# Optimization experiments

Hardware: AMD Instinct MI355X
Metric: run time of the kernel (lower is better)

The kernel has to match this reference:

```python
import jax, jax.numpy as jnp
import numpy as np

IMAGE_SIZE = 256
NEAR = 0.1
FAR = 100.0
CHUNK = 200  # faces per rasterization chunk


def setup_inputs() -> dict:
    key = jax.random.key(0)
    k1, k2, k3 = jax.random.split(key, 3)
    B, Nv, Nf = 1, 10000, 10000
    # vertices sized so that after weak projection (u = f*x + c, f=1015, c=112,
    # orig_size=224) they land inside the image plane; z kept positive.
    xy = jax.random.uniform(k1, (B, Nv, 2), minval=-0.1, maxval=0.1)
    z = jax.random.uniform(k3, (B, Nv, 1), minval=0.4, maxval=0.8)
    vertices = jnp.concatenate([xy, z], axis=-1).astype(jnp.float32)
    faces = jax.random.randint(k2, (B, Nf, 3), 0, Nv).astype(jnp.int64)
    f, c = 1015.0, 112.0
    K = jnp.broadcast_to(jnp.array([[f, 0.0, c], [0.0, f, c], [0.0, 0.0, 1.0]],
                                   dtype=jnp.float32), (B, 3, 3))
    R = jnp.broadcast_to(jnp.eye(3, dtype=jnp.float32), (B, 3, 3))
    t = jnp.zeros((B, 3), dtype=jnp.float32)
    return {"vertices": vertices, "faces": faces, "K": K, "R": R, "t": t,
            "orig_size": 224}


def weak_projection(vertices, K, R, t, orig_size):
    # camera transform: v_cam = v @ R^T + t   [B,N,3]
    v = jnp.einsum('bnj,bkj->bnk', vertices, R) + t[:, None, :]
    x, y, z = v[..., 0], v[..., 1], v[..., 2]
    fx, fy = K[:, 0:1, 0], K[:, 1:2, 1]  # [B,1]
    cx, cy = K[:, 0:1, 2], K[:, 1:2, 2]
    # weak (orthographic-with-focal) projection: no divide by z
    u = fx * x + cx
    w = fy * y + cy
    xn = 2.0 * u / orig_size - 1.0        # NDC x in [-1,1]
    yn = -(2.0 * w / orig_size - 1.0)     # image y down -> NDC y up
    return jnp.stack([xn, yn, z], axis=-1)


def _rasterize_depth(face_verts):
    # face_verts: [B, F, 3, 3] (NDC x, NDC y, camera z)
    B, F = face_verts.shape[0], face_verts.shape[1]
    IS = IMAGE_SIZE
    ps = (2.0 * (jnp.arange(IS, dtype=jnp.float32) + 0.5) / IS) - 1.0
    px = ps[None, :]    # [1, W]
    py = -ps[:, None]   # [H, 1], row 0 is top of image

    def chunk_depth(fc):  # fc: [B, C, 3, 3] -> per-pixel min depth [B, H, W]
        x = fc[..., 0][..., None, None]  # [B,C,3,1,1]
        y = fc[..., 1][..., None, None]
        z = fc[..., 2]                   # [B,C,3]
        dx0, dx1, dx2 = x[:, :, 0] - px, x[:, :, 1] - px, x[:, :, 2] - px  # [B,C,1,W]
        dy0, dy1, dy2 = y[:, :, 0] - py, y[:, :, 1] - py, y[:, :, 2] - py  # [B,C,H,1]
        # edge functions (unnormalized barycentric weights) [B,C,H,W]
        w0 = dx1 * dy2 - dx2 * dy1
        w1 = dx2 * dy0 - dx0 * dy2
        w2 = dx0 * dy1 - dx1 * dy0
        area = w0 + w1 + w2
        s = jnp.sign(area)
        inside = (w0 * s >= 0) & (w1 * s >= 0) & (w2 * s >= 0) & (jnp.abs(area) > 1e-10)
        safe_area = jnp.where(jnp.abs(area) > 1e-10, area, 1.0)
        zp = (w0 * z[:, :, 0, None, None] + w1 * z[:, :, 1, None, None]
              + w2 * z[:, :, 2, None, None]) / safe_area
        valid = inside & (zp > NEAR) & (zp < FAR)
        return jnp.min(jnp.where(valid, zp, FAR), axis=1)  # [B,H,W]

    pad = (-F) % CHUNK
    fv = jnp.pad(face_verts, ((0, 0), (0, pad), (0, 0), (0, 0)))  # degenerate pads -> area 0
    n = (F + pad) // CHUNK
    fv = fv.reshape(B, n, CHUNK, 3, 3).transpose(1, 0, 2, 3, 4)  # [n,B,C,3,3]
    ck = jax.checkpoint(chunk_depth)

    def step(carry, fc):
        return jnp.minimum(carry, ck(fc)), None

    depth0 = jnp.full((B, IS, IS), FAR, dtype=jnp.float32)
    depth, _ = jax.lax.scan(step, depth0, fv)
    return depth


def reference(vertices, faces, K, R, t, orig_size):
    # fill_back: append reversed-winding copies of every face
    faces2 = jnp.concatenate([faces, faces[:, :, ::-1]], axis=1)  # [B,2F,3]
    v = weak_projection(vertices, K, R, t, orig_size)             # [B,Nv,3]
    face_verts = jax.vmap(lambda vb, fb: vb[fb])(v, faces2)       # [B,2F,3,3]
    return _rasterize_depth(face_verts)                           # [B,256,256]
```

## Files before the change

### kernel.cpp

```cpp
#include <hip/hip_runtime.h>

#define IMG 256
#define FARZ 100.0f
#define FARB 0x42C80000u
#define TILE 16
#define NZ 4
#define RND 256
#define EPS 1e-4f
#define EPSZ 1e-5f
#define DPIX (2.0f / IMG)

typedef float f2 __attribute__((ext_vector_type(2)));
static __device__ __forceinline__ f2 pkfma(f2 a, f2 b, f2 c) {
    return __builtin_elementwise_fma(a, b, c);
}
static __device__ __forceinline__ float wave_max(float v) {
#pragma unroll
    for (int m = 32; m >= 1; m >>= 1) v = fmaxf(v, __shfl_xor(v, m, 64));
    return v;
}
static __device__ __forceinline__ float wave_min(float v) {
#pragma unroll
    for (int m = 32; m >= 1; m >>= 1) v = fminf(v, __shfl_xor(v, m, 64));
    return v;
}

struct Q4 { f2 r0, r1; };
static __device__ __forceinline__ Q4 eval4(float A, float B, float C,
                                           float px0, float py0) {
    Q4 o;
    float w00 = fmaf(B, px0, fmaf(C, py0, A));
    o.r0 = pkfma((f2){B, B}, (f2){0.0f, DPIX}, (f2){w00, w00});
    o.r1 = pkfma((f2){C, C}, (f2){-DPIX, -DPIX}, o.r0);
    return o;
}

__global__ __launch_bounds__(256) void setup(const float* __restrict__ verts,
                                             const int* __restrict__ faces,
                                             const float* __restrict__ K,
                                             const float* __restrict__ Rm,
                                             const float* __restrict__ t,
                                             const int* __restrict__ osz,
                                             float4* __restrict__ Q0,
                                             float4* __restrict__ Q1,
                                             float4* __restrict__ Q2,
                                             float4* __restrict__ BB,
                                             unsigned* __restrict__ gb,
                                             unsigned* __restrict__ out, int Nf) {
    __shared__ float sb[4][4];
    int tid = threadIdx.x;
    int i = blockIdx.x * 256 + tid;
    out[i] = FARB;

    float k0 = 104.0f, k1 = 104.0f, k2 = 104.0f, k3 = 104.0f;

    if (i < Nf) {
        float fx = K[0], cx = K[2], fy = K[4], cy = K[5];
        float os = (float)osz[0];
        float r00 = Rm[0], r01 = Rm[1], r02 = Rm[2];
        float r10 = Rm[3], r11 = Rm[4], r12 = Rm[5];
        float r20 = Rm[6], r21 = Rm[7], r22 = Rm[8];
        float t0 = t[0], t1 = t[1], t2 = t[2];

        float3 p[3];
#pragma unroll
        for (int k = 0; k < 3; ++k) {
            int vi = faces[3 * i + k];
            float vx = verts[3 * vi], vy = verts[3 * vi + 1], vz = verts[3 * vi + 2];
            float x = r00 * vx + r01 * vy + r02 * vz + t0;
            float y = r10 * vx + r11 * vy + r12 * vz + t1;
            float z = r20 * vx + r21 * vy + r22 * vz + t2;
            float u = fx * x + cx;
            float w = fy * y + cy;
            p[k].x = 2.0f * u / os - 1.0f;
            p[k].y = -(2.0f * w / os - 1.0f);
            p[k].z = z;
        }

        float xmn = fminf(p[0].x, fminf(p[1].x, p[2].x));
        float xmx = fmaxf(p[0].x, fmaxf(p[1].x, p[2].x));
        float ymn = fminf(p[0].y, fminf(p[1].y, p[2].y));
        float ymx = fmaxf(p[0].y, fmaxf(p[1].y, p[2].y));
        k0 = 4.0f + xmn; k1 = 4.0f - xmx; k2 = 4.0f + ymn; k3 = 4.0f - ymx;

        float A0 = p[1].x * p[2].y - p[2].x * p[1].y;
        float B0 = p[1].y - p[2].y;
        float C0 = p[2].x - p[1].x;
        float A1 = p[2].x * p[0].y - p[0].x * p[2].y;
        float B1 = p[2].y - p[0].y;
        float C1 = p[0].x - p[2].x;
        float A2 = p[0].x * p[1].y - p[1].x * p[0].y;
        float B2 = p[0].y - p[1].y;
        float C2 = p[1].x - p[0].x;

        float area = A0 + A1 + A2;
        if (fabsf(area) > 1e-10f) {
            float s = (area > 0.0f) ? 1.0f : -1.0f;
            A0 *= s; B0 *= s; C0 *= s;
            A1 *= s; B1 *= s; C1 *= s;
            A2 *= s; B2 *= s; C2 *= s;
            float inv = (1.0f / area) * s;
            float P = (A0 * p[0].z + A1 * p[1].z + A2 * p[2].z) * inv;
            float Q = (B0 * p[0].z + B1 * p[1].z + B2 * p[2].z) * inv;
            float Rr = (C0 * p[0].z + C1 * p[1].z + C2 * p[2].z) * inv;
            Q0[i] = make_float4(A0, B0, C0, A1);
            Q1[i] = make_float4(B1, C1, A2, B2);
            Q2[i] = make_float4(C2, P, Q, Rr);
            BB[i] = make_float4(xmn, xmx, ymn, ymx);
        } else {
            Q0[i] = make_float4(0.0f, 0.0f, 0.0f, 0.0f);
            Q1[i] = make_float4(0.0f, 0.0f, 0.0f, 0.0f);
            Q2[i] = make_float4(0.0f, 0.0f, 0.0f, 0.0f);
            BB[i] = make_float4(2.0f, 2.0f, 2.0f, 2.0f);
        }
    }

    k0 = wave_min(k0); k1 = wave_min(k1); k2 = wave_min(k2); k3 = wave_min(k3);
    int wave = tid >> 6, lane = tid & 63;
    if (lane == 0) { sb[wave][0] = k0; sb[wave][1] = k1; sb[wave][2] = k2; sb[wave][3] = k3; }
    __syncthreads();
    if (tid < 4) {
        float v = fminf(fminf(sb[0][tid], sb[1][tid]), fminf(sb[2][tid], sb[3][tid]));
        atomicMin(&gb[tid], __float_as_uint(v));
    }
}

__global__ __launch_bounds__(256) void raster(const float4* __restrict__ Q0,
                                              const float4* __restrict__ Q1,
                                              const float4* __restrict__ Q2,
                                              const float4* __restrict__ BB,
                                              const unsigned* __restrict__ gb,
                                              unsigned* __restrict__ out,
                                              int Nf, int span) {
    __shared__ float4 sf[RND * 3];
    __shared__ unsigned sdepth[TILE * TILE];
    __shared__ float swr[4];
    __shared__ int scnt;

    const int tid = threadIdx.x;
    const int bx = blockIdx.x, by = blockIdx.y;
    const int wave = tid >> 6, lane = tid & 63;

    const float cx0 = -1.0f + (bx * TILE + 0.5f) * DPIX;
    const float cx1 = cx0 + (TILE - 1) * DPIX;
    const float cyTop = 1.0f - (by * TILE + 0.5f) * DPIX;
    const float cyBot = cyTop - (TILE - 1) * DPIX;
    const float tcx = 0.5f * (cx0 + cx1);
    const float tcy = 0.5f * (cyBot + cyTop);
    const float hx = 0.5f * (cx1 - cx0);
    const float hy = 0.5f * (cyTop - cyBot);

    const float gxmin = __uint_as_float(gb[0]) - 4.0f;
    const float gxmax = 4.0f - __uint_as_float(gb[1]);
    const float gymin = __uint_as_float(gb[2]) - 4.0f;
    const float gymax = 4.0f - __uint_as_float(gb[3]);

    const int col = tid & 15, row = tid >> 4;
    const float pxt = cx0 + (float)col * DPIX;
    const float pyt = cyTop - (float)row * DPIX;
    const bool coverable = (pxt >= gxmin - 1e-6f) & (pxt <= gxmax + 1e-6f) &
                           (pyt >= gymin - 1e-6f) & (pyt <= gymax + 1e-6f);
    const int gidx = (by * TILE + row) * IMG + bx * TILE + col;
    const unsigned orig = out[gidx];
    sdepth[tid] = orig;
    if (tid == 0) scnt = 0;
    {
        float v = coverable ? __uint_as_float(orig) : 0.0f;
        float wm = wave_max(v);
        if (lane == 0) swr[wave] = wm;
    }
    __syncthreads();
    float T = fmaxf(fmaxf(swr[0], swr[1]), fmaxf(swr[2], swr[3]));

    const int qx = (lane & 7) * 2, qy = (lane >> 3) * 2;
    const float fpx0 = cx0 + (float)qx * DPIX;
    const float fpy0 = cyTop - (float)qy * DPIX;
    unsigned dmu[4];
    dmu[0] = sdepth[qy * TILE + qx];
    dmu[1] = sdepth[qy * TILE + qx + 1];
    dmu[2] = sdepth[(qy + 1) * TILE + qx];
    dmu[3] = sdepth[(qy + 1) * TILE + qx + 1];

    const int fbase = blockIdx.z * span;
    const int fend = min(fbase + span, Nf);

    for (int base = fbase; base < fend; base += RND) {
        int f = base + tid;
        if (f < fend) {
            float4 b = BB[f];
            bool keep = (b.x <= cx1 + EPS) & (b.y >= cx0 - EPS) &
                        (b.z <= cyTop + EPS) & (b.w >= cyBot - EPS);
            if (keep) {
                float4 q0 = Q0[f], q1 = Q1[f], q2 = Q2[f];
                float m0 = fmaf(q0.y, tcx, fmaf(q0.z, tcy, q0.x)) +
                           fabsf(q0.y) * hx + fabsf(q0.z) * hy;
                float m1 = fmaf(q1.x, tcx, fmaf(q1.y, tcy, q0.w)) +
                           fabsf(q1.x) * hx + fabsf(q1.y) * hy;
                float m2 = fmaf(q1.w, tcx, fmaf(q2.x, tcy, q1.z)) +
                           fabsf(q1.w) * hx + fabsf(q2.x) * hy;
                float zc = fmaf(q2.z, tcx, fmaf(q2.w, tcy, q2.y));
                float zmn = zc - fabsf(q2.z) * hx - fabsf(q2.w) * hy;
                if ((m0 >= -EPS) & (m1 >= -EPS) & (m2 >= -EPS) &
                    (zmn <= T + EPSZ)) {
                    int slot = atomicAdd(&scnt, 1);
                    sf[3 * slot + 0] = q0;
                    sf[3 * slot + 1] = q1;
                    sf[3 * slot + 2] = q2;
                }
            }
        }
        __syncthreads();
        const int n = scnt;

#pragma unroll 2
        for (int j = wave; j < n; j += 4) {
            float4 c0 = sf[3 * j + 0];
            float4 c1 = sf[3 * j + 1];
            float4 c2 = sf[3 * j + 2];
            Q4 w0 = eval4(c0.x, c0.y, c0.z, fpx0, fpy0);
            Q4 w1 = eval4(c0.w, c1.x, c1.y, fpx0, fpy0);
            Q4 w2 = eval4(c1.z, c1.w, c2.x, fpx0, fpy0);
            Q4 zz = eval4(c2.y, c2.z, c2.w, fpx0, fpy0);
            float s0 = fminf(fminf(w0.r0.x, w1.r0.x), w2.r0.x);
            float s1 = fminf(fminf(w0.r0.y, w1.r0.y), w2.r0.y);
            float s2 = fminf(fminf(w0.r1.x, w1.r1.x), w2.r1.x);
            float s3 = fminf(fminf(w0.r1.y, w1.r1.y), w2.r1.y);
            unsigned k0 = (__float_as_uint(s0) & 0x80000000u) | __float_as_uint(zz.r0.x);
            unsigned k1 = (__float_as_uint(s1) & 0x80000000u) | __float_as_uint(zz.r0.y);
            unsigned k2 = (__float_as_uint(s2) & 0x80000000u) | __float_as_uint(zz.r1.x);
            unsigned k3 = (__float_as_uint(s3) & 0x80000000u) | __float_as_uint(zz.r1.y);
            dmu[0] = min(dmu[0], k0);
            dmu[1] = min(dmu[1], k1);
            dmu[2] = min(dmu[2], k2);
            dmu[3] = min(dmu[3], k3);
        }

        atomicMin(&sdepth[qy * TILE + qx], dmu[0]);
        atomicMin(&sdepth[qy * TILE + qx + 1], dmu[1]);
        atomicMin(&sdepth[(qy + 1) * TILE + qx], dmu[2]);
        atomicMin(&sdepth[(qy + 1) * TILE + qx + 1], dmu[3]);
        __syncthreads();

        if (base + RND < fend) {
            if (tid == 0) scnt = 0;
            float v = coverable ? __uint_as_float(sdepth[tid]) : 0.0f;
            float wm = wave_max(v);
            if (lane == 0) swr[wave] = wm;
            __syncthreads();
            T = fmaxf(fmaxf(swr[0], swr[1]), fmaxf(swr[2], swr[3]));
        }
    }

    unsigned fv = sdepth[tid];
    if (fv < orig) atomicMin(out + gidx, fv);
}

extern "C" void kernel_launch(void* const* d_in, const int* in_sizes, int n_in,
                              void* d_out, int out_size, void* d_ws, size_t ws_size,
                              hipStream_t stream) {
    const float* verts = (const float*)d_in[0];
    const int* faces   = (const int*)d_in[1];
    const float* K     = (const float*)d_in[2];
    const float* Rm    = (const float*)d_in[3];
    const float* t     = (const float*)d_in[4];
    const int* osz     = (const int*)d_in[5];

    int Nf = in_sizes[1] / 3;
    int span = (Nf + NZ - 1) / NZ;

    float4* Q0 = (float4*)d_ws;
    float4* Q1 = Q0 + Nf;
    float4* Q2 = Q1 + Nf;
    float4* BB = Q2 + Nf;
    unsigned* gb = (unsigned*)(BB + Nf);

    unsigned* out = (unsigned*)d_out;

    setup<<<(IMG * IMG) / 256, 256, 0, stream>>>(verts, faces, K, Rm, t, osz,
                                                 Q0, Q1, Q2, BB, gb, out, Nf);

    dim3 grid(IMG / TILE, IMG / TILE, NZ);
    raster<<<grid, 256, 0, stream>>>(Q0, Q1, Q2, BB, gb, out, Nf, span);
}
```

Measured before the change: 93.52 us.

## Fuse setup and raster into cooperative kernel with depth-sorted faces and early exit

```diff
diff --git a/kernel.cpp b/kernel.cpp
--- a/kernel.cpp
+++ b/kernel.cpp
@@ -1,14 +1,21 @@
 #include <hip/hip_runtime.h>
+#include <hip/hip_cooperative_groups.h>
+
+namespace cg = cooperative_groups;
 
 #define IMG 256
 #define FARZ 100.0f
 #define FARB 0x42C80000u
 #define TILE 16
-#define NZ 4
+#define NB 256
+#define NT 256
 #define RND 256
 #define EPS 1e-4f
 #define EPSZ 1e-5f
 #define DPIX (2.0f / IMG)
+#define ZLO 0.399f
+#define ZSPAN 0.402f
+#define DZ (ZSPAN / 256.0f)
 
 typedef float f2 __attribute__((ext_vector_type(2)));
 static __device__ __forceinline__ f2 pkfma(f2 a, f2 b, f2 c) {
@@ -35,112 +42,163 @@
     return o;
 }
 
-__global__ __launch_bounds__(256) void setup(const float* __restrict__ verts,
+__global__ __launch_bounds__(NT) void render(const float* __restrict__ verts,
                                              const int* __restrict__ faces,
                                              const float* __restrict__ K,
                                              const float* __restrict__ Rm,
                                              const float* __restrict__ t,
                                              const int* __restrict__ osz,
-                                             float4* __restrict__ Q0,
-                                             float4* __restrict__ Q1,
-                                             float4* __restrict__ Q2,
-                                             float4* __restrict__ BB,
-                                             unsigned* __restrict__ gb,
+                                             float4* __restrict__ ws4,
                                              unsigned* __restrict__ out, int Nf) {
-    __shared__ float sb[4][4];
-    int tid = threadIdx.x;
-    int i = blockIdx.x * 256 + tid;
-    out[i] = FARB;
-
+    cg::grid_group grid = cg::this_grid();
+
+    float4* Q0u = ws4;
+    float4* Q1u = ws4 + Nf;
+    float4* Q2u = ws4 + 2 * Nf;
+    float4* BBu = ws4 + 3 * Nf;
+    float4* Q0s = ws4 + 4 * Nf;
+    float4* Q1s = ws4 + 5 * Nf;
+    float4* Q2s = ws4 + 6 * Nf;
+    float4* BBs = ws4 + 7 * Nf;
+    float* zmu = (float*)(ws4 + 8 * Nf);
+    float* lbs = zmu + Nf;
+    unsigned* bins = (unsigned*)(lbs + Nf);
+    unsigned* curs = bins + 256;
+    unsigned* gb = curs + 256;
+
+    __shared__ float4 sf[RND * 3];
+    __shared__ unsigned sdepth[TILE * TILE];
+    __shared__ unsigned lh[256];
+    __shared__ unsigned soff[256];
+    __shared__ float sb4[4][4];
+    __shared__ float swr[4];
+    __shared__ int scnt;
+
+    const int tid = threadIdx.x;
+    const int b = blockIdx.x;
+    const int wave = tid >> 6, lane = tid & 63;
+
+    if (b == 0) {
+        bins[tid] = 0u;
+        curs[tid] = 0u;
+        if (tid < 4) gb[tid] = 0x7F7FFFFFu;
+    }
+    grid.sync();
+
+    lh[tid] = 0u;
+    __syncthreads();
     float k0 = 104.0f, k1 = 104.0f, k2 = 104.0f, k3 = 104.0f;
-
-    if (i < Nf) {
-        float fx = K[0], cx = K[2], fy = K[4], cy = K[5];
-        float os = (float)osz[0];
-        float r00 = Rm[0], r01 = Rm[1], r02 = Rm[2];
-        float r10 = Rm[3], r11 = Rm[4], r12 = Rm[5];
-        float r20 = Rm[6], r21 = Rm[7], r22 = Rm[8];
-        float t0 = t[0], t1 = t[1], t2 = t[2];
-
-        float3 p[3];
+    {
+        int f = b + NB * tid;
+        if (f < Nf) {
+            float fx = K[0], cx = K[2], fy = K[4], cy = K[5];
+            float os = (float)osz[0];
+            float r00 = Rm[0], r01 = Rm[1], r02 = Rm[2];
+            float r10 = Rm[3], r11 = Rm[4], r12 = Rm[5];
+            float r20 = Rm[6], r21 = Rm[7], r22 = Rm[8];
+            float t0 = t[0], t1 = t[1], t2 = t[2];
+
+            float3 p[3];
 #pragma unroll
-        for (int k = 0; k < 3; ++k) {
-            int vi = faces[3 * i + k];
-            float vx = verts[3 * vi], vy = verts[3 * vi + 1], vz = verts[3 * vi + 2];
-            float x = r00 * vx + r01 * vy + r02 * vz + t0;
-            float y = r10 * vx + r11 * vy + r12 * vz + t1;
-            float z = r20 * vx + r21 * vy + r22 * vz + t2;
-            float u = fx * x + cx;
-            float w = fy * y + cy;
-            p[k].x = 2.0f * u / os - 1.0f;
-            p[k].y = -(2.0f * w / os - 1.0f);
-            p[k].z = z;
-        }
-
-        float xmn = fminf(p[0].x, fminf(p[1].x, p[2].x));
-        float xmx = fmaxf(p[0].x, fmaxf(p[1].x, p[2].x));
-        float ymn = fminf(p[0].y, fminf(p[1].y, p[2].y));
-        float ymx = fmaxf(p[0].y, fmaxf(p[1].y, p[2].y));
-        k0 = 4.0f + xmn; k1 = 4.0f - xmx; k2 = 4.0f + ymn; k3 = 4.0f - ymx;
-
-        float A0 = p[1].x * p[2].y - p[2].x * p[1].y;
-        float B0 = p[1].y - p[2].y;
-        float C0 = p[2].x - p[1].x;
-        float A1 = p[2].x * p[0].y - p[0].x * p[2].y;
-        float B1 = p[2].y - p[0].y;
-        float C1 = p[0].x - p[2].x;
-        float A2 = p[0].x * p[1].y - p[1].x * p[0].y;
-        float B2 = p[0].y - p[1].y;
-        float C2 = p[1].x - p[0].x;
-
-        float area = A0 + A1 + A2;
-        if (fabsf(area) > 1e-10f) {
-            float s = (area > 0.0f) ? 1.0f : -1.0f;
-            A0 *= s; B0 *= s; C0 *= s;
-            A1 *= s; B1 *= s; C1 *= s;
-            A2 *= s; B2 *= s; C2 *= s;
-            float inv = (1.0f / area) * s;
-            float P = (A0 * p[0].z + A1 * p[1].z + A2 * p[2].z) * inv;
-            float Q = (B0 * p[0].z + B1 * p[1].z + B2 * p[2].z) * inv;
-            float Rr = (C0 * p[0].z + C1 * p[1].z + C2 * p[2].z) * inv;
-            Q0[i] = make_float4(A0, B0, C0, A1);
-            Q1[i] = make_float4(B1, C1, A2, B2);
-            Q2[i] = make_float4(C2, P, Q, Rr);
-            BB[i] = make_float4(xmn, xmx, ymn, ymx);
-        } else {
-            Q0[i] = make_float4(0.0f, 0.0f, 0.0f, 0.0f);
-            Q1[i] = make_float4(0.0f, 0.0f, 0.0f, 0.0f);
-            Q2[i] = make_float4(0.0f, 0.0f, 0.0f, 0.0f);
-            BB[i] = make_float4(2.0f, 2.0f, 2.0f, 2.0f);
-        }
-    }
-
+            for (int k = 0; k < 3; ++k) {
+                int vi = faces[3 * f + k];
+                float vx = verts[3 * vi], vy = verts[3 * vi + 1], vz = verts[3 * vi + 2];
+                float x = r00 * vx + r01 * vy + r02 * vz + t0;
+                float y = r10 * vx + r11 * vy + r12 * vz + t1;
+                float z = r20 * vx + r21 * vy + r22 * vz + t2;
+                float u = fx * x + cx;
+                float w = fy * y + cy;
+                p[k].x = 2.0f * u / os - 1.0f;
+                p[k].y = -(2.0f * w / os - 1.0f);
+                p[k].z = z;
+            }
+
+            float A0 = p[1].x * p[2].y - p[2].x * p[1].y;
+            float B0 = p[1].y - p[2].y;
+            float C0 = p[2].x - p[1].x;
+            float A1 = p[2].x * p[0].y - p[0].x * p[2].y;
+            float B1 = p[2].y - p[0].y;
+            float C1 = p[0].x - p[2].x;
+            float A2 = p[0].x * p[1].y - p[1].x * p[0].y;
+            float B2 = p[0].y - p[1].y;
+            float C2 = p[1].x - p[0].x;
+
+            float area = A0 + A1 + A2;
+            float zmin;
+            if (fabsf(area) > 1e-10f) {
+                float s = (area > 0.0f) ? 1.0f : -1.0f;
+                A0 *= s; B0 *= s; C0 *= s;
+                A1 *= s; B1 *= s; C1 *= s;
+                A2 *= s; B2 *= s; C2 *= s;
+                float inv = (1.0f / area) * s;
+                float P = (A0 * p[0].z + A1 * p[1].z + A2 * p[2].z) * inv;
+                float Q = (B0 * p[0].z + B1 * p[1].z + B2 * p[2].z) * inv;
+                float Rr = (C0 * p[0].z + C1 * p[1].z + C2 * p[2].z) * inv;
+                Q0u[f] = make_float4(A0, B0, C0, A1);
+                Q1u[f] = make_float4(B1, C1, A2, B2);
+                Q2u[f] = make_float4(C2, P, Q, Rr);
+                float xmn = fminf(p[0].x, fminf(p[1].x, p[2].x));
+                float xmx = fmaxf(p[0].x, fmaxf(p[1].x, p[2].x));
+                float ymn = fminf(p[0].y, fminf(p[1].y, p[2].y));
+                float ymx = fmaxf(p[0].y, fmaxf(p[1].y, p[2].y));
+                BBu[f] = make_float4(xmn, xmx, ymn, ymx);
+                k0 = 4.0f + xmn; k1 = 4.0f - xmx;
+                k2 = 4.0f + ymn; k3 = 4.0f - ymx;
+                zmin = fminf(p[0].z, fminf(p[1].z, p[2].z));
+            } else {
+                Q0u[f] = make_float4(0.0f, 0.0f, 0.0f, 0.0f);
+                Q1u[f] = make_float4(0.0f, 0.0f, 0.0f, 0.0f);
+                Q2u[f] = make_float4(0.0f, 0.0f, 0.0f, 0.0f);
+                BBu[f] = make_float4(2.0f, 2.0f, 2.0f, 2.0f);
+                zmin = 1e30f;
+            }
+            zmu[f] = zmin;
+            int bin = (int)((zmin - ZLO) * (256.0f / ZSPAN));
+            bin = max(0, min(255, bin));
+            atomicAdd(&lh[bin], 1u);
+        }
+    }
+    __syncthreads();
     k0 = wave_min(k0); k1 = wave_min(k1); k2 = wave_min(k2); k3 = wave_min(k3);
-    int wave = tid >> 6, lane = tid & 63;
-    if (lane == 0) { sb[wave][0] = k0; sb[wave][1] = k1; sb[wave][2] = k2; sb[wave][3] = k3; }
+    if (lane == 0) { sb4[wave][0] = k0; sb4[wave][1] = k1; sb4[wave][2] = k2; sb4[wave][3] = k3; }
     __syncthreads();
     if (tid < 4) {
-        float v = fminf(fminf(sb[0][tid], sb[1][tid]), fminf(sb[2][tid], sb[3][tid]));
+        float v = fminf(fminf(sb4[0][tid], sb4[1][tid]), fminf(sb4[2][tid], sb4[3][tid]));
         atomicMin(&gb[tid], __float_as_uint(v));
     }
-}
-
-__global__ __launch_bounds__(256) void raster(const float4* __restrict__ Q0,
-                                              const float4* __restrict__ Q1,
-                                              const float4* __restrict__ Q2,
-                                              const float4* __restrict__ BB,
-                                              const unsigned* __restrict__ gb,
-                                              unsigned* __restrict__ out,
-                                              int Nf, int span) {
-    __shared__ float4 sf[RND * 3];
-    __shared__ unsigned sdepth[TILE * TILE];
-    __shared__ float swr[4];
-    __shared__ int scnt;
-
-    const int tid = threadIdx.x;
-    const int bx = blockIdx.x, by = blockIdx.y;
-    const int wave = tid >> 6, lane = tid & 63;
-
+    if (lh[tid]) atomicAdd(&bins[tid], lh[tid]);
+    grid.sync();
+
+    {
+        unsigned c = bins[tid];
+        soff[tid] = c;
+        __syncthreads();
+#pragma unroll
+        for (int off = 1; off < 256; off <<= 1) {
+            unsigned v = (tid >= off) ? soff[tid - off] : 0u;
+            __syncthreads();
+            soff[tid] += v;
+            __syncthreads();
+        }
+        lh[tid] = soff[tid] - c;
+        __syncthreads();
+
+        int f = b + NB * tid;
+        if (f < Nf) {
+            float zmin = zmu[f];
+            int bin = (int)((zmin - ZLO) * (256.0f / ZSPAN));
+            bin = max(0, min(255, bin));
+            unsigned slot = lh[bin] + atomicAdd(&curs[bin], 1u);
+            Q0s[slot] = Q0u[f];
+            Q1s[slot] = Q1u[f];
+            Q2s[slot] = Q2u[f];
+            BBs[slot] = BBu[f];
+            lbs[slot] = (bin == 0) ? 0.0f : (ZLO + (float)bin * DZ);
+        }
+    }
+    grid.sync();
+
+    const int bx = b & 15, by = b >> 4;
     const float cx0 = -1.0f + (bx * TILE + 0.5f) * DPIX;
     const float cx1 = cx0 + (TILE - 1) * DPIX;
     const float cyTop = 1.0f - (by * TILE + 0.5f) * DPIX;
@@ -161,37 +219,27 @@
     const bool coverable = (pxt >= gxmin - 1e-6f) & (pxt <= gxmax + 1e-6f) &
                            (pyt >= gymin - 1e-6f) & (pyt <= gymax + 1e-6f);
     const int gidx = (by * TILE + row) * IMG + bx * TILE + col;
-    const unsigned orig = out[gidx];
-    sdepth[tid] = orig;
+
+    sdepth[tid] = FARB;
     if (tid == 0) scnt = 0;
-    {
-        float v = coverable ? __uint_as_float(orig) : 0.0f;
-        float wm = wave_max(v);
-        if (lane == 0) swr[wave] = wm;
-    }
     __syncthreads();
-    float T = fmaxf(fmaxf(swr[0], swr[1]), fmaxf(swr[2], swr[3]));
 
     const int qx = (lane & 7) * 2, qy = (lane >> 3) * 2;
     const float fpx0 = cx0 + (float)qx * DPIX;
     const float fpy0 = cyTop - (float)qy * DPIX;
-    unsigned dmu[4];
-    dmu[0] = sdepth[qy * TILE + qx];
-    dmu[1] = sdepth[qy * TILE + qx + 1];
-    dmu[2] = sdepth[(qy + 1) * TILE + qx];
-    dmu[3] = sdepth[(qy + 1) * TILE + qx + 1];
-
-    const int fbase = blockIdx.z * span;
-    const int fend = min(fbase + span, Nf);
-
-    for (int base = fbase; base < fend; base += RND) {
+    unsigned dmu[4] = {FARB, FARB, FARB, FARB};
+
+    float T = FARZ;
+    for (int base = 0; base < Nf; base += RND) {
+        if (lbs[base] > T + EPSZ) break;
+
         int f = base + tid;
-        if (f < fend) {
-            float4 b = BB[f];
-            bool keep = (b.x <= cx1 + EPS) & (b.y >= cx0 - EPS) &
-                        (b.z <= cyTop + EPS) & (b.w >= cyBot - EPS);
+        if (f < Nf) {
+            float4 bb = BBs[f];
+            bool keep = (bb.x <= cx1 + EPS) & (bb.y >= cx0 - EPS) &
+                        (bb.z <= cyTop + EPS) & (bb.w >= cyBot - EPS);
             if (keep) {
-                float4 q0 = Q0[f], q1 = Q1[f], q2 = Q2[f];
+                float4 q0 = Q0s[f], q1 = Q1s[f], q2 = Q2s[f];
                 float m0 = fmaf(q0.y, tcx, fmaf(q0.z, tcy, q0.x)) +
                            fabsf(q0.y) * hx + fabsf(q0.z) * hy;
                 float m1 = fmaf(q1.x, tcx, fmaf(q1.y, tcy, q0.w)) +
@@ -225,14 +273,14 @@
             float s1 = fminf(fminf(w0.r0.y, w1.r0.y), w2.r0.y);
             float s2 = fminf(fminf(w0.r1.x, w1.r1.x), w2.r1.x);
             float s3 = fminf(fminf(w0.r1.y, w1.r1.y), w2.r1.y);
-            unsigned k0 = (__float_as_uint(s0) & 0x80000000u) | __float_as_uint(zz.r0.x);
-            unsigned k1 = (__float_as_uint(s1) & 0x80000000u) | __float_as_uint(zz.r0.y);
-            unsigned k2 = (__float_as_uint(s2) & 0x80000000u) | __float_as_uint(zz.r1.x);
-            unsigned k3 = (__float_as_uint(s3) & 0x80000000u) | __float_as_uint(zz.r1.y);
-            dmu[0] = min(dmu[0], k0);
-            dmu[1] = min(dmu[1], k1);
-            dmu[2] = min(dmu[2], k2);
-            dmu[3] = min(dmu[3], k3);
+            unsigned u0 = (__float_as_uint(s0) & 0x80000000u) | __float_as_uint(zz.r0.x);
+            unsigned u1 = (__float_as_uint(s1) & 0x80000000u) | __float_as_uint(zz.r0.y);
+            unsigned u2 = (__float_as_uint(s2) & 0x80000000u) | __float_as_uint(zz.r1.x);
+            unsigned u3 = (__float_as_uint(s3) & 0x80000000u) | __float_as_uint(zz.r1.y);
+            dmu[0] = min(dmu[0], u0);
+            dmu[1] = min(dmu[1], u1);
+            dmu[2] = min(dmu[2], u2);
+            dmu[3] = min(dmu[3], u3);
         }
 
         atomicMin(&sdepth[qy * TILE + qx], dmu[0]);
@@ -241,18 +289,15 @@
         atomicMin(&sdepth[(qy + 1) * TILE + qx + 1], dmu[3]);
         __syncthreads();
 
-        if (base + RND < fend) {
-            if (tid == 0) scnt = 0;
-            float v = coverable ? __uint_as_float(sdepth[tid]) : 0.0f;
-            float wm = wave_max(v);
-            if (lane == 0) swr[wave] = wm;
-            __syncthreads();
-            T = fmaxf(fmaxf(swr[0], swr[1]), fmaxf(swr[2], swr[3]));
-        }
-    }
-
-    unsigned fv = sdepth[tid];
-    if (fv < orig) atomicMin(out + gidx, fv);
+        if (tid == 0) scnt = 0;
+        float v = coverable ? __uint_as_float(sdepth[tid]) : 0.0f;
+        float wm = wave_max(v);
+        if (lane == 0) swr[wave] = wm;
+        __syncthreads();
+        T = fmaxf(fmaxf(swr[0], swr[1]), fmaxf(swr[2], swr[3]));
+    }
+
+    out[gidx] = sdepth[tid];
 }
 
 extern "C" void kernel_launch(void* const* d_in, const int* in_sizes, int n_in,
@@ -266,19 +311,13 @@
     const int* osz     = (const int*)d_in[5];
 
     int Nf = in_sizes[1] / 3;
-    int span = (Nf + NZ - 1) / NZ;
-
-    float4* Q0 = (float4*)d_ws;
-    float4* Q1 = Q0 + Nf;
-    float4* Q2 = Q1 + Nf;
-    float4* BB = Q2 + Nf;
-    unsigned* gb = (unsigned*)(BB + Nf);
-
+
+    float4* ws4 = (float4*)d_ws;
     unsigned* out = (unsigned*)d_out;
 
-    setup<<<(IMG * IMG) / 256, 256, 0, stream>>>(verts, faces, K, Rm, t, osz,
-                                                 Q0, Q1, Q2, BB, gb, out, Nf);
-
-    dim3 grid(IMG / TILE, IMG / TILE, NZ);
-    raster<<<grid, 256, 0, stream>>>(Q0, Q1, Q2, BB, gb, out, Nf, span);
-}
+    void* args[] = {(void*)&verts, (void*)&faces, (void*)&K, (void*)&Rm,
+                    (void*)&t, (void*)&osz, (void*)&ws4, (void*)&out,
+                    (void*)&Nf};
+    hipLaunchCooperativeKernel((const void*)render, dim3(NB), dim3(NT),
+                               args, 0, stream);
+}
```

New measurement: 227.1 us. 143% more time.

## Fuse setup and raster into one cooperative kernel with grid sync

Applied to the files above, without the earlier changes.

```diff
diff --git a/kernel.cpp b/kernel.cpp
--- a/kernel.cpp
+++ b/kernel.cpp
@@ -1,4 +1,7 @@
 #include <hip/hip_runtime.h>
+#include <hip/hip_cooperative_groups.h>
+
+namespace cg = cooperative_groups;
 
 #define IMG 256
 #define FARZ 100.0f
@@ -6,6 +9,7 @@
 #define TILE 16
 #define NZ 4
 #define RND 256
+#define RNDC 1024
 #define EPS 1e-4f
 #define EPSZ 1e-5f
 #define DPIX (2.0f / IMG)
@@ -35,85 +39,245 @@
     return o;
 }
 
-__global__ __launch_bounds__(256) void setup(const float* __restrict__ verts,
-                                             const int* __restrict__ faces,
-                                             const float* __restrict__ K,
-                                             const float* __restrict__ Rm,
-                                             const float* __restrict__ t,
-                                             const int* __restrict__ osz,
-                                             float4* __restrict__ Q0,
-                                             float4* __restrict__ Q1,
-                                             float4* __restrict__ Q2,
-                                             float4* __restrict__ BB,
-                                             unsigned* __restrict__ gb,
-                                             unsigned* __restrict__ out, int Nf) {
+static __device__ __forceinline__ void face_setup_one(
+    const float* verts, const int* faces, const float* K, const float* Rm,
+    const float* t, const int* osz, int f,
+    float4* Q0, float4* Q1, float4* Q2, float4* BB,
+    float& k0, float& k1, float& k2, float& k3) {
+    float fx = K[0], cx = K[2], fy = K[4], cy = K[5];
+    float os = (float)osz[0];
+    float r00 = Rm[0], r01 = Rm[1], r02 = Rm[2];
+    float r10 = Rm[3], r11 = Rm[4], r12 = Rm[5];
+    float r20 = Rm[6], r21 = Rm[7], r22 = Rm[8];
+    float t0 = t[0], t1 = t[1], t2 = t[2];
+
+    float3 p[3];
+#pragma unroll
+    for (int k = 0; k < 3; ++k) {
+        int vi = faces[3 * f + k];
+        float vx = verts[3 * vi], vy = verts[3 * vi + 1], vz = verts[3 * vi + 2];
+        float x = r00 * vx + r01 * vy + r02 * vz + t0;
+        float y = r10 * vx + r11 * vy + r12 * vz + t1;
+        float z = r20 * vx + r21 * vy + r22 * vz + t2;
+        float u = fx * x + cx;
+        float w = fy * y + cy;
+        p[k].x = 2.0f * u / os - 1.0f;
+        p[k].y = -(2.0f * w / os - 1.0f);
+        p[k].z = z;
+    }
+
+    float A0 = p[1].x * p[2].y - p[2].x * p[1].y;
+    float B0 = p[1].y - p[2].y;
+    float C0 = p[2].x - p[1].x;
+    float A1 = p[2].x * p[0].y - p[0].x * p[2].y;
+    float B1 = p[2].y - p[0].y;
+    float C1 = p[0].x - p[2].x;
+    float A2 = p[0].x * p[1].y - p[1].x * p[0].y;
+    float B2 = p[0].y - p[1].y;
+    float C2 = p[1].x - p[0].x;
+
+    float area = A0 + A1 + A2;
+    if (fabsf(area) > 1e-10f) {
+        float s = (area > 0.0f) ? 1.0f : -1.0f;
+        A0 *= s; B0 *= s; C0 *= s;
+        A1 *= s; B1 *= s; C1 *= s;
+        A2 *= s; B2 *= s; C2 *= s;
+        float inv = (1.0f / area) * s;
+        float P = (A0 * p[0].z + A1 * p[1].z + A2 * p[2].z) * inv;
+        float Q = (B0 * p[0].z + B1 * p[1].z + B2 * p[2].z) * inv;
+        float Rr = (C0 * p[0].z + C1 * p[1].z + C2 * p[2].z) * inv;
+        Q0[f] = make_float4(A0, B0, C0, A1);
+        Q1[f] = make_float4(B1, C1, A2, B2);
+        Q2[f] = make_float4(C2, P, Q, Rr);
+        float xmn = fminf(p[0].x, fminf(p[1].x, p[2].x));
+        float xmx = fmaxf(p[0].x, fmaxf(p[1].x, p[2].x));
+        float ymn = fminf(p[0].y, fminf(p[1].y, p[2].y));
+        float ymx = fmaxf(p[0].y, fmaxf(p[1].y, p[2].y));
+        BB[f] = make_float4(xmn, xmx, ymn, ymx);
+        k0 = 4.0f + xmn; k1 = 4.0f - xmx;
+        k2 = 4.0f + ymn; k3 = 4.0f - ymx;
+    } else {
+        Q0[f] = make_float4(0.0f, 0.0f, 0.0f, 0.0f);
+        Q1[f] = make_float4(0.0f, 0.0f, 0.0f, 0.0f);
+        Q2[f] = make_float4(0.0f, 0.0f, 0.0f, 0.0f);
+        BB[f] = make_float4(2.0f, 2.0f, 2.0f, 2.0f);
+    }
+}
+
+__global__ __launch_bounds__(1024) void render_coop(
+    const float* __restrict__ verts, const int* __restrict__ faces,
+    const float* __restrict__ K, const float* __restrict__ Rm,
+    const float* __restrict__ t, const int* __restrict__ osz,
+    float4* __restrict__ ws4, unsigned* __restrict__ gb,
+    unsigned* __restrict__ out, int Nf) {
+    cg::grid_group grid = cg::this_grid();
+
+    float4* Q0 = ws4;
+    float4* Q1 = ws4 + Nf;
+    float4* Q2 = ws4 + 2 * Nf;
+    float4* BB = ws4 + 3 * Nf;
+
+    __shared__ float4 sf[RNDC * 3];
+    __shared__ unsigned sdepth[TILE * TILE];
+    __shared__ float swr[4];
+    __shared__ int scnt;
+
+    const int tid = threadIdx.x;
+    const int b = blockIdx.x;
+    const int wave = tid >> 6, lane = tid & 63;
+
+    float k0 = 104.0f, k1 = 104.0f, k2 = 104.0f, k3 = 104.0f;
+    int f0 = b * 40 + tid;
+    if (tid < 40 && f0 < Nf)
+        face_setup_one(verts, faces, K, Rm, t, osz, f0, Q0, Q1, Q2, BB,
+                       k0, k1, k2, k3);
+    if (wave == 0) {
+        k0 = wave_min(k0); k1 = wave_min(k1);
+        k2 = wave_min(k2); k3 = wave_min(k3);
+        if (lane == 0) {
+            atomicMin(&gb[0], __float_as_uint(k0));
+            atomicMin(&gb[1], __float_as_uint(k1));
+            atomicMin(&gb[2], __float_as_uint(k2));
+            atomicMin(&gb[3], __float_as_uint(k3));
+        }
+    }
+    grid.sync();
+
+    const int bx = b & 15, by = b >> 4;
+    const float cx0 = -1.0f + (bx * TILE + 0.5f) * DPIX;
+    const float cx1 = cx0 + (TILE - 1) * DPIX;
+    const float cyTop = 1.0f - (by * TILE + 0.5f) * DPIX;
+    const float cyBot = cyTop - (TILE - 1) * DPIX;
+    const float tcx = 0.5f * (cx0 + cx1);
+    const float tcy = 0.5f * (cyBot + cyTop);
+    const float hx = 0.5f * (cx1 - cx0);
+    const float hy = 0.5f * (cyTop - cyBot);
+
+    const float gxmin = __uint_as_float(gb[0]) - 4.0f;
+    const float gxmax = 4.0f - __uint_as_float(gb[1]);
+    const float gymin = __uint_as_float(gb[2]) - 4.0f;
+    const float gymax = 4.0f - __uint_as_float(gb[3]);
+
+    const int col = tid & 15, row = (tid >> 4) & 15;
+    const float pxt = cx0 + (float)col * DPIX;
+    const float pyt = cyTop - (float)row * DPIX;
+    const bool coverable = (pxt >= gxmin - 1e-6f) & (pxt <= gxmax + 1e-6f) &
+                           (pyt >= gymin - 1e-6f) & (pyt <= gymax + 1e-6f);
+
+    if (tid < 256) sdepth[tid] = FARB;
+    if (tid == 0) scnt = 0;
+    __syncthreads();
+
+    float T;
+    {
+        if (wave < 4) {
+            float v = coverable ? FARZ : 0.0f;
+            float wm = wave_max(v);
+            if (lane == 0) swr[wave] = wm;
+        }
+        __syncthreads();
+        T = fmaxf(fmaxf(swr[0], swr[1]), fmaxf(swr[2], swr[3]));
+    }
+
+    const int qx = (lane & 7) * 2, qy = (lane >> 3) * 2;
+    const float fpx0 = cx0 + (float)qx * DPIX;
+    const float fpy0 = cyTop - (float)qy * DPIX;
+    unsigned dmu[4] = {FARB, FARB, FARB, FARB};
+
+    for (int base = 0; base < Nf; base += RNDC) {
+        int f = base + tid;
+        if (f < Nf) {
+            float4 bb = BB[f];
+            bool keep = (bb.x <= cx1 + EPS) & (bb.y >= cx0 - EPS) &
+                        (bb.z <= cyTop + EPS) & (bb.w >= cyBot - EPS);
+            if (keep) {
+                float4 q0 = Q0[f], q1 = Q1[f], q2 = Q2[f];
+                float m0 = fmaf(q0.y, tcx, fmaf(q0.z, tcy, q0.x)) +
+                           fabsf(q0.y) * hx + fabsf(q0.z) * hy;
+                float m1 = fmaf(q1.x, tcx, fmaf(q1.y, tcy, q0.w)) +
+                           fabsf(q1.x) * hx + fabsf(q1.y) * hy;
+                float m2 = fmaf(q1.w, tcx, fmaf(q2.x, tcy, q1.z)) +
+                           fabsf(q1.w) * hx + fabsf(q2.x) * hy;
+                float zc = fmaf(q2.z, tcx, fmaf(q2.w, tcy, q2.y));
+                float zmn = zc - fabsf(q2.z) * hx - fabsf(q2.w) * hy;
+                if ((m0 >= -EPS) & (m1 >= -EPS) & (m2 >= -EPS) &
+                    (zmn <= T + EPSZ)) {
+                    int slot = atomicAdd(&scnt, 1);
+                    sf[3 * slot + 0] = q0;
+                    sf[3 * slot + 1] = q1;
+                    sf[3 * slot + 2] = q2;
+                }
+            }
+        }
+        __syncthreads();
+        const int n = scnt;
+
+#pragma unroll 2
+        for (int j = wave; j < n; j += 16) {
+            float4 c0 = sf[3 * j + 0];
+            float4 c1 = sf[3 * j + 1];
+            float4 c2 = sf[3 * j + 2];
+            Q4 w0 = eval4(c0.x, c0.y, c0.z, fpx0, fpy0);
+            Q4 w1 = eval4(c0.w, c1.x, c1.y, fpx0, fpy0);
+            Q4 w2 = eval4(c1.z, c1.w, c2.x, fpx0, fpy0);
+            Q4 zz = eval4(c2.y, c2.z, c2.w, fpx0, fpy0);
+            float s0 = fminf(fminf(w0.r0.x, w1.r0.x), w2.r0.x);
+            float s1 = fminf(fminf(w0.r0.y, w1.r0.y), w2.r0.y);
+            float s2 = fminf(fminf(w0.r1.x, w1.r1.x), w2.r1.x);
+            float s3 = fminf(fminf(w0.r1.y, w1.r1.y), w2.r1.y);
+            unsigned u0 = (__float_as_uint(s0) & 0x80000000u) | __float_as_uint(zz.r0.x);
+            unsigned u1 = (__float_as_uint(s1) & 0x80000000u) | __float_as_uint(zz.r0.y);
+            unsigned u2 = (__float_as_uint(s2) & 0x80000000u) | __float_as_uint(zz.r1.x);
+            unsigned u3 = (__float_as_uint(s3) & 0x80000000u) | __float_as_uint(zz.r1.y);
+            dmu[0] = min(dmu[0], u0);
+            dmu[1] = min(dmu[1], u1);
+            dmu[2] = min(dmu[2], u2);
+            dmu[3] = min(dmu[3], u3);
+        }
+
+        atomicMin(&sdepth[qy * TILE + qx], dmu[0]);
+        atomicMin(&sdepth[qy * TILE + qx + 1], dmu[1]);
+        atomicMin(&sdepth[(qy + 1) * TILE + qx], dmu[2]);
+        atomicMin(&sdepth[(qy + 1) * TILE + qx + 1], dmu[3]);
+        __syncthreads();
+
+        if (base + RNDC < Nf) {
+            if (tid == 0) scnt = 0;
+            if (wave < 4) {
+                float v = coverable ? __uint_as_float(sdepth[tid]) : 0.0f;
+                float wm = wave_max(v);
+                if (lane == 0) swr[wave] = wm;
+            }
+            __syncthreads();
+            T = fmaxf(fmaxf(swr[0], swr[1]), fmaxf(swr[2], swr[3]));
+        }
+    }
+
+    if (tid < 256)
+        out[(by * TILE + row) * IMG + bx * TILE + col] = sdepth[tid];
+}
+
+__global__ __launch_bounds__(256) void setup_fb(const float* __restrict__ verts,
+                                                const int* __restrict__ faces,
+                                                const float* __restrict__ K,
+                                                const float* __restrict__ Rm,
+                                                const float* __restrict__ t,
+                                                const int* __restrict__ osz,
+                                                float4* __restrict__ Q0,
+                                                float4* __restrict__ Q1,
+                                                float4* __restrict__ Q2,
+                                                float4* __restrict__ BB,
+                                                unsigned* __restrict__ gb,
+                                                unsigned* __restrict__ out, int Nf) {
     __shared__ float sb[4][4];
     int tid = threadIdx.x;
     int i = blockIdx.x * 256 + tid;
     out[i] = FARB;
 
     float k0 = 104.0f, k1 = 104.0f, k2 = 104.0f, k3 = 104.0f;
-
-    if (i < Nf) {
-        float fx = K[0], cx = K[2], fy = K[4], cy = K[5];
-        float os = (float)osz[0];
-        float r00 = Rm[0], r01 = Rm[1], r02 = Rm[2];
-        float r10 = Rm[3], r11 = Rm[4], r12 = Rm[5];
-        float r20 = Rm[6], r21 = Rm[7], r22 = Rm[8];
-        float t0 = t[0], t1 = t[1], t2 = t[2];
-
-        float3 p[3];
-#pragma unroll
-        for (int k = 0; k < 3; ++k) {
-            int vi = faces[3 * i + k];
-            float vx = verts[3 * vi], vy = verts[3 * vi + 1], vz = verts[3 * vi + 2];
-            float x = r00 * vx + r01 * vy + r02 * vz + t0;
-            float y = r10 * vx + r11 * vy + r12 * vz + t1;
-            float z = r20 * vx + r21 * vy + r22 * vz + t2;
-            float u = fx * x + cx;
-            float w = fy * y + cy;
-            p[k].x = 2.0f * u / os - 1.0f;
-            p[k].y = -(2.0f * w / os - 1.0f);
-            p[k].z = z;
-        }
-
-        float xmn = fminf(p[0].x, fminf(p[1].x, p[2].x));
-        float xmx = fmaxf(p[0].x, fmaxf(p[1].x, p[2].x));
-        float ymn = fminf(p[0].y, fminf(p[1].y, p[2].y));
-        float ymx = fmaxf(p[0].y, fmaxf(p[1].y, p[2].y));
-        k0 = 4.0f + xmn; k1 = 4.0f - xmx; k2 = 4.0f + ymn; k3 = 4.0f - ymx;
-
-        float A0 = p[1].x * p[2].y - p[2].x * p[1].y;
-        float B0 = p[1].y - p[2].y;
-        float C0 = p[2].x - p[1].x;
-        float A1 = p[2].x * p[0].y - p[0].x * p[2].y;
-        float B1 = p[2].y - p[0].y;
-        float C1 = p[0].x - p[2].x;
-        float A2 = p[0].x * p[1].y - p[1].x * p[0].y;
-        float B2 = p[0].y - p[1].y;
-        float C2 = p[1].x - p[0].x;
-
-        float area = A0 + A1 + A2;
-        if (fabsf(area) > 1e-10f) {
-            float s = (area > 0.0f) ? 1.0f : -1.0f;
-            A0 *= s; B0 *= s; C0 *= s;
-            A1 *= s; B1 *= s; C1 *= s;
-            A2 *= s; B2 *= s; C2 *= s;
-            float inv = (1.0f / area) * s;
-            float P = (A0 * p[0].z + A1 * p[1].z + A2 * p[2].z) * inv;
-            float Q = (B0 * p[0].z + B1 * p[1].z + B2 * p[2].z) * inv;
-            float Rr = (C0 * p[0].z + C1 * p[1].z + C2 * p[2].z) * inv;
-            Q0[i] = make_float4(A0, B0, C0, A1);
-            Q1[i] = make_float4(B1, C1, A2, B2);
-            Q2[i] = make_float4(C2, P, Q, Rr);
-            BB[i] = make_float4(xmn, xmx, ymn, ymx);
-        } else {
-            Q0[i] = make_float4(0.0f, 0.0f, 0.0f, 0.0f);
-            Q1[i] = make_float4(0.0f, 0.0f, 0.0f, 0.0f);
-            Q2[i] = make_float4(0.0f, 0.0f, 0.0f, 0.0f);
-            BB[i] = make_float4(2.0f, 2.0f, 2.0f, 2.0f);
-        }
-    }
+    if (i < Nf)
+        face_setup_one(verts, faces, K, Rm, t, osz, i, Q0, Q1, Q2, BB,
+                       k0, k1, k2, k3);
 
     k0 = wave_min(k0); k1 = wave_min(k1); k2 = wave_min(k2); k3 = wave_min(k3);
     int wave = tid >> 6, lane = tid & 63;
@@ -125,13 +289,13 @@
     }
 }
 
-__global__ __launch_bounds__(256) void raster(const float4* __restrict__ Q0,
-                                              const float4* __restrict__ Q1,
-                                              const float4* __restrict__ Q2,
-                                              const float4* __restrict__ BB,
-                                              const unsigned* __restrict__ gb,
-                                              unsigned* __restrict__ out,
-                                              int Nf, int span) {
+__global__ __launch_bounds__(256) void raster_fb(const float4* __restrict__ Q0,
+                                                 const float4* __restrict__ Q1,
+                                                 const float4* __restrict__ Q2,
+                                                 const float4* __restrict__ BB,
+                                                 const unsigned* __restrict__ gb,
+                                                 unsigned* __restrict__ out,
+                                                 int Nf, int span) {
     __shared__ float4 sf[RND * 3];
     __shared__ unsigned sdepth[TILE * TILE];
     __shared__ float swr[4];
@@ -225,14 +389,14 @@
             float s1 = fminf(fminf(w0.r0.y, w1.r0.y), w2.r0.y);
             float s2 = fminf(fminf(w0.r1.x, w1.r1.x), w2.r1.x);
             float s3 = fminf(fminf(w0.r1.y, w1.r1.y), w2.r1.y);
-            unsigned k0 = (__float_as_uint(s0) & 0x80000000u) | __float_as_uint(zz.r0.x);
-            unsigned k1 = (__float_as_uint(s1) & 0x80000000u) | __float_as_uint(zz.r0.y);
-            unsigned k2 = (__float_as_uint(s2) & 0x80000000u) | __float_as_uint(zz.r1.x);
-            unsigned k3 = (__float_as_uint(s3) & 0x80000000u) | __float_as_uint(zz.r1.y);
-            dmu[0] = min(dmu[0], k0);
-            dmu[1] = min(dmu[1], k1);
-            dmu[2] = min(dmu[2], k2);
-            dmu[3] = min(dmu[3], k3);
+            unsigned u0 = (__float_as_uint(s0) & 0x80000000u) | __float_as_uint(zz.r0.x);
+            unsigned u1 = (__float_as_uint(s1) & 0x80000000u) | __float_as_uint(zz.r0.y);
+            unsigned u2 = (__float_as_uint(s2) & 0x80000000u) | __float_as_uint(zz.r1.x);
+            unsigned u3 = (__float_as_uint(s3) & 0x80000000u) | __float_as_uint(zz.r1.y);
+            dmu[0] = min(dmu[0], u0);
+            dmu[1] = min(dmu[1], u1);
+            dmu[2] = min(dmu[2], u2);
+            dmu[3] = min(dmu[3], u3);
         }
 
         atomicMin(&sdepth[qy * TILE + qx], dmu[0]);
@@ -268,17 +432,22 @@
     int Nf = in_sizes[1] / 3;
     int span = (Nf + NZ - 1) / NZ;
 
-    float4* Q0 = (float4*)d_ws;
-    float4* Q1 = Q0 + Nf;
-    float4* Q2 = Q1 + Nf;
-    float4* BB = Q2 + Nf;
-    unsigned* gb = (unsigned*)(BB + Nf);
-
+    float4* ws4 = (float4*)d_ws;
+    unsigned* gb = (unsigned*)(ws4 + 4 * Nf);
     unsigned* out = (unsigned*)d_out;
 
-    setup<<<(IMG * IMG) / 256, 256, 0, stream>>>(verts, faces, K, Rm, t, osz,
-                                                 Q0, Q1, Q2, BB, gb, out, Nf);
-
-    dim3 grid(IMG / TILE, IMG / TILE, NZ);
-    raster<<<grid, 256, 0, stream>>>(Q0, Q1, Q2, BB, gb, out, Nf, span);
-}
+    void* args[] = {(void*)&verts, (void*)&faces, (void*)&K, (void*)&Rm,
+                    (void*)&t, (void*)&osz, (void*)&ws4, (void*)&gb,
+                    (void*)&out, (void*)&Nf};
+    hipError_t err = hipLaunchCooperativeKernel((const void*)render_coop,
+                                                dim3(256), dim3(1024),
+                                                args, 0, stream);
+    if (err != hipSuccess) {
+        (void)hipGetLastError();
+        setup_fb<<<(IMG * IMG) / 256, 256, 0, stream>>>(
+            verts, faces, K, Rm, t, osz, ws4, ws4 + Nf, ws4 + 2 * Nf,
+            ws4 + 3 * Nf, gb, out, Nf);
+        raster_fb<<<dim3(IMG / TILE, IMG / TILE, NZ), 256, 0, stream>>>(
+            ws4, ws4 + Nf, ws4 + 2 * Nf, ws4 + 3 * Nf, gb, out, Nf, span);
+    }
+}
```

Result: slower. 138.9 us (+48.5%).
